# Kernel optimization log

Measured on AMD Instinct MI355X. Metric: run time of the kernel, lower is better.

The kernel has to match this reference:

```python
import jax, jax.numpy as jnp
import numpy as np

HIDDEN = 2048
N_HEADS = 16
N_KV = 4
HEAD_DIM = 128
THETA = 500000.0
FREQ_ALLOC = 20  # t section; h = w = (HEAD_DIM//2 - 20)//2 = 22
T = 2048


def setup_inputs() -> dict:
    key = jax.random.key(0)
    k1, k2, k3, k4 = jax.random.split(key, 4)
    positions = jax.random.randint(k1, (3, T), 0, 1024, dtype=jnp.int32)
    hidden_states = jax.random.normal(k2, (T, HIDDEN), dtype=jnp.float32)
    w_qkv = jax.random.normal(k3, (HIDDEN, (N_HEADS + 2 * N_KV) * HEAD_DIM), dtype=jnp.float32) * 0.02
    w_o = jax.random.normal(k4, (N_HEADS * HEAD_DIM, HIDDEN), dtype=jnp.float32) * 0.02
    return {"positions": positions, "hidden_states": hidden_states, "w_qkv": w_qkv, "w_o": w_o}


def _mrope_cos_sin(positions):
    # standard rope table evaluated at positions: cos/sin each [3, T, HEAD_DIM//2]
    inv_freq = 1.0 / (THETA ** (jnp.arange(0, HEAD_DIM, 2, dtype=jnp.float32) / HEAD_DIM))
    freqs = positions.astype(jnp.float32)[..., None] * inv_freq
    cos, sin = jnp.cos(freqs), jnp.sin(freqs)
    sh = (HEAD_DIM // 2 - FREQ_ALLOC) // 2  # 22

    def section(c):
        c_t = c[0, :, -FREQ_ALLOC:]          # time dims from t-positions
        c_h = c[1, :, 0:2 * sh:2]            # even low-freq dims from h-positions
        c_w = c[2, :, 1:2 * sh:2]            # odd low-freq dims from w-positions
        c_hw = jnp.stack([c_h, c_w], axis=-1).reshape(c_h.shape[0], 2 * sh)
        return jnp.concatenate([c_hw, c_t], axis=-1)  # [T, HEAD_DIM//2]

    return section(cos), section(sin)


def _rotate_interleaved(x, cos, sin):
    # is_neox_style=False: even/odd interleaved rotation. x: [T, H, HEAD_DIM]
    x1, x2 = x[..., 0::2], x[..., 1::2]
    c, s = cos[:, None, :], sin[:, None, :]
    o1 = x1 * c - x2 * s
    o2 = x2 * c + x1 * s
    return jnp.stack([o1, o2], axis=-1).reshape(x.shape)


def reference(positions, hidden_states, w_qkv, w_o):
    q_size = N_HEADS * HEAD_DIM
    kv_size = N_KV * HEAD_DIM
    qkv = hidden_states @ w_qkv  # [T, 3072]
    q = qkv[:, :q_size].reshape(T, N_HEADS, HEAD_DIM)
    k = qkv[:, q_size:q_size + kv_size].reshape(T, N_KV, HEAD_DIM)
    v = qkv[:, q_size + kv_size:].reshape(T, N_KV, HEAD_DIM)

    cos, sin = _mrope_cos_sin(positions)
    q = _rotate_interleaved(q, cos, sin)
    k = _rotate_interleaved(k, cos, sin)

    # GQA causal attention
    rep = N_HEADS // N_KV
    kr = jnp.repeat(k, rep, axis=1)  # [T, N_HEADS, D]
    vr = jnp.repeat(v, rep, axis=1)
    scale = HEAD_DIM ** -0.5
    scores = jnp.einsum('qhd,khd->hqk', q, kr) * scale
    causal = jnp.tril(jnp.ones((T, T), dtype=bool))
    scores = jnp.where(causal[None], scores, jnp.finfo(scores.dtype).min)
    attn = jax.nn.softmax(scores, axis=-1)
    out = jnp.einsum('hqk,khd->qhd', attn, vr).reshape(T, N_HEADS * HEAD_DIM)
    return out @ w_o
```

## Files before the change

kernel.cpp:

```cpp
#include <hip/hip_runtime.h>
#include <math.h>

#define T 2048
#define HIDDEN 2048
#define NH 16
#define NKV 4
#define HD 128
#define QKV_N 3072
#define Q_SIZE 2048
#define KV_SIZE 512

typedef __attribute__((ext_vector_type(8))) short short8;
typedef __attribute__((ext_vector_type(4))) short short4v;
typedef __attribute__((ext_vector_type(4))) float floatx4;

__device__ __forceinline__ unsigned short f2bf(float f) {
    union { float f; unsigned int u; } v; v.f = f;
    unsigned int u = v.u;
    u += 0x7fffu + ((u >> 16) & 1u);
    return (unsigned short)(u >> 16);
}

__device__ __forceinline__ void gload_lds16(const unsigned short* g, unsigned short* l) {
    __builtin_amdgcn_global_load_lds((const __attribute__((address_space(1))) unsigned int*)g,
                                     (__attribute__((address_space(3))) unsigned int*)l, 16, 0, 0);
}

__global__ __launch_bounds__(256) void prep_misc(const float* __restrict__ hidden,
                                                 const float* __restrict__ w_qkv,
                                                 const float* __restrict__ w_o,
                                                 const int* __restrict__ positions,
                                                 unsigned short* __restrict__ hb,
                                                 unsigned short* __restrict__ wqt,
                                                 unsigned short* __restrict__ wot,
                                                 float* __restrict__ cosT,
                                                 float* __restrict__ sinT) {
    __shared__ float tile[32][33];
    const int b = blockIdx.x;
    const int tid = threadIdx.x;
    const int tx = tid & 31, ty = tid >> 5;

    if (b < 4096) {
        int i = (b * 256 + tid) * 4;
        float4 v = *(const float4*)(hidden + i);
        hb[i]     = f2bf(v.x);
        hb[i + 1] = f2bf(v.y);
        hb[i + 2] = f2bf(v.z);
        hb[i + 3] = f2bf(v.w);
    } else if (b < 10240) {
        int idx = b - 4096;
        int c0 = (idx % 96) * 32, r0 = (idx / 96) * 32;
#pragma unroll
        for (int i = 0; i < 4; ++i)
            tile[ty + i * 8][tx] = w_qkv[(long)(r0 + ty + i * 8) * QKV_N + c0 + tx];
        __syncthreads();
#pragma unroll
        for (int i = 0; i < 4; ++i)
            wqt[(long)(c0 + ty + i * 8) * HIDDEN + r0 + tx] = f2bf(tile[tx][ty + i * 8]);
    } else if (b < 14336) {
        int idx = b - 10240;
        int c0 = (idx % 64) * 32, r0 = (idx / 64) * 32;
#pragma unroll
        for (int i = 0; i < 4; ++i)
            tile[ty + i * 8][tx] = w_o[(long)(r0 + ty + i * 8) * HIDDEN + c0 + tx];
        __syncthreads();
#pragma unroll
        for (int i = 0; i < 4; ++i)
            wot[(long)(c0 + ty + i * 8) * HIDDEN + r0 + tx] = f2bf(tile[tx][ty + i * 8]);
    } else {
        int idx = b - 14336;
        int t = idx * 4 + (tid >> 6);
        int j = tid & 63;
        int row = (j >= 44) ? 0 : ((j & 1) ? 2 : 1);
        int pos = positions[row * T + t];
        float invf = exp2f((float)j * -0.29580571f);
        float ang = (float)pos * invf;
        cosT[t * 64 + j] = cosf(ang);
        sinT[t * 64 + j] = sinf(ang);
    }
}

__global__ __launch_bounds__(256) void gemm_qkv(const unsigned short* __restrict__ A,
                                                const unsigned short* __restrict__ B,
                                                const float* __restrict__ cosT,
                                                const float* __restrict__ sinT,
                                                unsigned short* __restrict__ qb,
                                                unsigned short* __restrict__ kb,
                                                unsigned short* __restrict__ vt) {
    __shared__ __align__(16) unsigned short As[2][64 * 64];
    __shared__ __align__(16) unsigned short Bs[2][128 * 64];
    const int K = HIDDEN;
    const int tid = threadIdx.x;
    const int wv = tid >> 6;
    const int lane = tid & 63;
    const int m = lane & 15, qd = lane >> 4;
    const unsigned short* Ab = A + (long)(blockIdx.x * 64) * K;
    const unsigned short* Bb = B + (long)(blockIdx.y * 128) * K;

    floatx4 acc[4][2];
#pragma unroll
    for (int i = 0; i < 4; ++i)
#pragma unroll
        for (int j = 0; j < 2; ++j) acc[i][j] = (floatx4){0.f, 0.f, 0.f, 0.f};

#define QKV_STAGE(buf, k0)                                                                   \
    do {                                                                                     \
        _Pragma("unroll") for (int i_ = 0; i_ < 2; ++i_) {                                   \
            int s_ = i_ * 256 + tid, r_ = s_ >> 3, c_ = (s_ & 7) ^ (r_ & 7);                 \
            gload_lds16(Ab + (long)r_ * K + (k0) + c_ * 8, &As[buf][i_ * 2048 + wv * 512]);  \
        }                                                                                    \
        _Pragma("unroll") for (int i_ = 0; i_ < 4; ++i_) {                                   \
            int s_ = i_ * 256 + tid, r_ = s_ >> 3, c_ = (s_ & 7) ^ (r_ & 7);                 \
            gload_lds16(Bb + (long)r_ * K + (k0) + c_ * 8, &Bs[buf][i_ * 2048 + wv * 512]);  \
        }                                                                                    \
    } while (0)

    QKV_STAGE(0, 0);
    int cur = 0;
    for (int k0 = 0; k0 < K; k0 += 64) {
        __syncthreads();
        if (k0 + 64 < K) QKV_STAGE(cur ^ 1, k0 + 64);
#pragma unroll
        for (int kk = 0; kk < 2; ++kk) {
            const int rch = ((kk * 4 + qd) ^ (m & 7)) * 8;
            short8 a[4], b[2];
#pragma unroll
            for (int i = 0; i < 4; ++i) a[i] = *(const short8*)&As[cur][(i * 16 + m) * 64 + rch];
#pragma unroll
            for (int j = 0; j < 2; ++j) b[j] = *(const short8*)&Bs[cur][(wv * 32 + j * 16 + m) * 64 + rch];
#pragma unroll
            for (int i = 0; i < 4; ++i)
#pragma unroll
                for (int j = 0; j < 2; ++j)
                    acc[i][j] = __builtin_amdgcn_mfma_f32_16x16x32_bf16(a[i], b[j], acc[i][j], 0, 0, 0);
        }
        cur ^= 1;
    }
#undef QKV_STAGE

    const int by = blockIdx.y;
    if (by < 20) {
        const float sgn = (m & 1) ? 1.f : -1.f;
        const float qscale = 0.08838834764831845f;
#pragma unroll
        for (int i = 0; i < 4; ++i) {
#pragma unroll
            for (int r = 0; r < 4; ++r) {
                const int t = blockIdx.x * 64 + i * 16 + qd * 4 + r;
                const float* ct = cosT + t * 64;
                const float* st = sinT + t * 64;
#pragma unroll
                for (int j = 0; j < 2; ++j) {
                    const int cq = wv * 32 + j * 16 + m;
                    const int j2 = cq >> 1;
                    float val = acc[i][j][r];
                    float prt = __shfl_xor(val, 1);
                    float o = val * ct[j2] + sgn * prt * st[j2];
                    const int col = by * 128 + cq;
                    if (by < 16) qb[(long)t * Q_SIZE + col] = f2bf(o * qscale);
                    else         kb[(long)t * KV_SIZE + (col - 2048)] = f2bf(o);
                }
            }
        }
    } else {
        const int g = by - 20;
#pragma unroll
        for (int i = 0; i < 4; ++i)
#pragma unroll
            for (int j = 0; j < 2; ++j) {
                const int d = wv * 32 + j * 16 + m;
                const int t0 = blockIdx.x * 64 + i * 16 + qd * 4;
                unsigned short o4[4];
#pragma unroll
                for (int r = 0; r < 4; ++r) o4[r] = f2bf(acc[i][j][r]);
                *(short4v*)&vt[((long)g * HD + d) * T + t0] = *(short4v*)o4;
            }
    }
}

__global__ __launch_bounds__(256) void gemm_out(const unsigned short* __restrict__ A,
                                                const unsigned short* __restrict__ B,
                                                float* __restrict__ C,
                                                int K, int ldc) {
    __shared__ __align__(16) unsigned short As[2][64 * 64];
    __shared__ __align__(16) unsigned short Bs[2][128 * 64];
    const int tid = threadIdx.x;
    const int wv = tid >> 6;
    const int lane = tid & 63;
    const int m = lane & 15, qd = lane >> 4;
    const unsigned short* Ab = A + (long)(blockIdx.x * 64) * K;
    const unsigned short* Bb = B + (long)(blockIdx.y * 128) * K;

    floatx4 acc[4][2];
#pragma unroll
    for (int i = 0; i < 4; ++i)
#pragma unroll
        for (int j = 0; j < 2; ++j) acc[i][j] = (floatx4){0.f, 0.f, 0.f, 0.f};

#define OUT_STAGE(buf, k0)                                                                   \
    do {                                                                                     \
        _Pragma("unroll") for (int i_ = 0; i_ < 2; ++i_) {                                   \
            int s_ = i_ * 256 + tid, r_ = s_ >> 3, c_ = (s_ & 7) ^ (r_ & 7);                 \
            gload_lds16(Ab + (long)r_ * K + (k0) + c_ * 8, &As[buf][i_ * 2048 + wv * 512]);  \
        }                                                                                    \
        _Pragma("unroll") for (int i_ = 0; i_ < 4; ++i_) {                                   \
            int s_ = i_ * 256 + tid, r_ = s_ >> 3, c_ = (s_ & 7) ^ (r_ & 7);                 \
            gload_lds16(Bb + (long)r_ * K + (k0) + c_ * 8, &Bs[buf][i_ * 2048 + wv * 512]);  \
        }                                                                                    \
    } while (0)

    OUT_STAGE(0, 0);
    int cur = 0;
    for (int k0 = 0; k0 < K; k0 += 64) {
        __syncthreads();
        if (k0 + 64 < K) OUT_STAGE(cur ^ 1, k0 + 64);
#pragma unroll
        for (int kk = 0; kk < 2; ++kk) {
            const int rch = ((kk * 4 + qd) ^ (m & 7)) * 8;
            short8 a[4], b[2];
#pragma unroll
            for (int i = 0; i < 4; ++i) a[i] = *(const short8*)&As[cur][(i * 16 + m) * 64 + rch];
#pragma unroll
            for (int j = 0; j < 2; ++j) b[j] = *(const short8*)&Bs[cur][(wv * 32 + j * 16 + m) * 64 + rch];
#pragma unroll
            for (int i = 0; i < 4; ++i)
#pragma unroll
                for (int j = 0; j < 2; ++j)
                    acc[i][j] = __builtin_amdgcn_mfma_f32_16x16x32_bf16(a[i], b[j], acc[i][j], 0, 0, 0);
        }
        cur ^= 1;
    }
#undef OUT_STAGE

#pragma unroll
    for (int i = 0; i < 4; ++i)
#pragma unroll
        for (int j = 0; j < 2; ++j)
#pragma unroll
            for (int r = 0; r < 4; ++r)
                C[(long)(blockIdx.x * 64 + i * 16 + qd * 4 + r) * ldc +
                  blockIdx.y * 128 + wv * 32 + j * 16 + m] = acc[i][j][r];
}

__global__ __launch_bounds__(256, 2) void flash_attn(const unsigned short* __restrict__ qb,
                                                     const unsigned short* __restrict__ kb,
                                                     const unsigned short* __restrict__ vt,
                                                     float* __restrict__ Opart,
                                                     float* __restrict__ MLpart) {
    __shared__ __align__(16) unsigned short Kbuf[2][64 * 128];
    __shared__ __align__(16) unsigned short Vbuf[128 * 64];
    __shared__ __align__(16) unsigned short Pls[4][32 * 72];

    const int tid = threadIdx.x;
    const int wv = tid >> 6;
    const int lane = tid & 63;
    const int m = lane & 15;
    const int qd = lane >> 4;

    const int bx = blockIdx.x;
    const int c_ = bx & 255;
    const int hi = bx >> 8;
    const int h = c_ >> 4;
    const int j_ = c_ & 15;
    const int qt = hi ? (j_ >> 1) : (15 - (j_ >> 1));
    const int half = j_ & 1;
    const int g = h >> 2;
    unsigned short* myP = Pls[wv];

    const int n0 = qt + 1;
    const int jt0 = half ? n0 : 0;
    const int jt1 = half ? 2 * qt + 2 : n0;
    const int q0 = qt * 128;

    short8 aq[2][4];
#pragma unroll
    for (int s = 0; s < 2; ++s)
#pragma unroll
        for (int kk = 0; kk < 4; ++kk)
            aq[s][kk] = *(const short8*)(qb + (long)(q0 + s * 64 + wv * 16 + m) * Q_SIZE +
                                         h * HD + kk * 32 + qd * 8);

    floatx4 acc_o[2][8];
#pragma unroll
    for (int s = 0; s < 2; ++s)
#pragma unroll
        for (int nb = 0; nb < 8; ++nb) acc_o[s][nb] = (floatx4){0.f, 0.f, 0.f, 0.f};
    float mrow[2] = {-1e30f, -1e30f};
    float lrow[2] = {0.f, 0.f};

#pragma unroll
    for (int i = 0; i < 4; ++i) {
        int s_ = i * 256 + tid;
        int r = s_ >> 4, c = (s_ & 15) ^ (r & 15);
        gload_lds16(kb + (long)(jt0 * 64 + r) * KV_SIZE + g * HD + c * 8,
                    &Kbuf[0][i * 2048 + wv * 512]);
    }
    int cur = 0;
    for (int jt = jt0; jt < jt1; ++jt) {
        __syncthreads();

        if (jt + 1 < jt1) {
#pragma unroll
            for (int i = 0; i < 4; ++i) {
                int s_ = i * 256 + tid;
                int r = s_ >> 4, c = (s_ & 15) ^ (r & 15);
                gload_lds16(kb + (long)((jt + 1) * 64 + r) * KV_SIZE + g * HD + c * 8,
                            &Kbuf[cur ^ 1][i * 2048 + wv * 512]);
            }
        }
#pragma unroll
        for (int i = 0; i < 4; ++i) {
            int s_ = i * 256 + tid;
            int r = s_ >> 3, c = (s_ & 7) ^ (r & 7);
            gload_lds16(vt + ((long)g * HD + r) * T + jt * 64 + c * 8,
                        &Vbuf[i * 2048 + wv * 512]);
        }

        floatx4 acc_s[2][4];
#pragma unroll
        for (int s = 0; s < 2; ++s)
#pragma unroll
            for (int c = 0; c < 4; ++c) acc_s[s][c] = (floatx4){0.f, 0.f, 0.f, 0.f};
#pragma unroll
        for (int kk = 0; kk < 4; ++kk) {
#pragma unroll
            for (int c = 0; c < 4; ++c) {
                short8 ak = *(const short8*)&Kbuf[cur][(c * 16 + m) * 128 +
                                                       (((4 * kk + qd) ^ m) * 8)];
                acc_s[0][c] = __builtin_amdgcn_mfma_f32_16x16x32_bf16(ak, aq[0][kk], acc_s[0][c], 0, 0, 0);
                acc_s[1][c] = __builtin_amdgcn_mfma_f32_16x16x32_bf16(ak, aq[1][kk], acc_s[1][c], 0, 0, 0);
            }
        }

#pragma unroll
        for (int s = 0; s < 2; ++s) {
            const int dg = 2 * qt + s;
            if (jt >= dg) {
                const bool full = (jt > dg);
#pragma unroll
                for (int c = 0; c < 4; ++c)
#pragma unroll
                    for (int r = 0; r < 4; ++r)
                        if (full || (c * 16 + qd * 4 + r > wv * 16 + m)) acc_s[s][c][r] = -1e30f;
            }
            float mx = acc_s[s][0][0];
#pragma unroll
            for (int c = 0; c < 4; ++c)
#pragma unroll
                for (int r = 0; r < 4; ++r) mx = fmaxf(mx, acc_s[s][c][r]);
            mx = fmaxf(mx, __shfl_xor(mx, 16));
            mx = fmaxf(mx, __shfl_xor(mx, 32));
            float mnew = fmaxf(mrow[s], mx);
            float alpha = __expf(mrow[s] - mnew);
            mrow[s] = mnew;

            float pv[4][4];
            float lsum = 0.f;
#pragma unroll
            for (int c = 0; c < 4; ++c)
#pragma unroll
                for (int r = 0; r < 4; ++r) {
                    pv[c][r] = __expf(acc_s[s][c][r] - mnew);
                    lsum += pv[c][r];
                }
            lsum += __shfl_xor(lsum, 16);
            lsum += __shfl_xor(lsum, 32);
            lrow[s] = lrow[s] * alpha + lsum;
#pragma unroll
            for (int nb = 0; nb < 8; ++nb)
#pragma unroll
                for (int r = 0; r < 4; ++r) acc_o[s][nb][r] *= alpha;
#pragma unroll
            for (int c = 0; c < 4; ++c) {
                short4v pk = {(short)f2bf(pv[c][0]), (short)f2bf(pv[c][1]),
                              (short)f2bf(pv[c][2]), (short)f2bf(pv[c][3])};
                *(short4v*)&myP[(s * 16 + m) * 72 + c * 16 + qd * 4] = pk;
            }
        }

        __syncthreads();

#pragma unroll
        for (int kk = 0; kk < 2; ++kk) {
            short8 pa0 = *(const short8*)&myP[m * 72 + kk * 32 + qd * 8];
            short8 pa1 = *(const short8*)&myP[(16 + m) * 72 + kk * 32 + qd * 8];
#pragma unroll
            for (int nb = 0; nb < 8; ++nb) {
                short8 av = *(const short8*)&Vbuf[(nb * 16 + m) * 64 +
                                                  (((4 * kk + qd) ^ (m & 7)) * 8)];
                acc_o[0][nb] = __builtin_amdgcn_mfma_f32_16x16x32_bf16(av, pa0, acc_o[0][nb], 0, 0, 0);
                acc_o[1][nb] = __builtin_amdgcn_mfma_f32_16x16x32_bf16(av, pa1, acc_o[1][nb], 0, 0, 0);
            }
        }
        cur ^= 1;
    }

    const int unit = (h * 16 + qt) * 2 + half;
#pragma unroll
    for (int s = 0; s < 2; ++s) {
        const long rb = (long)unit * 128 + s * 64 + wv * 16 + m;
#pragma unroll
        for (int nb = 0; nb < 8; ++nb)
            *(floatx4*)&Opart[rb * 128 + nb * 16 + qd * 4] = acc_o[s][nb];
        if (qd == 0) {
            MLpart[rb * 2]     = mrow[s];
            MLpart[rb * 2 + 1] = lrow[s];
        }
    }
}

__global__ __launch_bounds__(256) void attn_combine(const float* __restrict__ Opart,
                                                    const float* __restrict__ MLpart,
                                                    unsigned short* __restrict__ ab) {
    const int tid = threadIdx.x;
    const int q = blockIdx.x * 16 + (tid >> 4);
    const int h = blockIdx.y;
    const int d0 = (tid & 15) * 8;
    const int qt = q >> 7, lr = q & 127;
    const long r0 = ((long)(h * 16 + qt) * 2) * 128 + lr;
    const long r1 = r0 + 128;
    float m0 = MLpart[r0 * 2], l0 = MLpart[r0 * 2 + 1];
    float m1 = MLpart[r1 * 2], l1 = MLpart[r1 * 2 + 1];
    float M = fmaxf(m0, m1);
    float a0 = __expf(m0 - M), a1 = __expf(m1 - M);
    float inv = 1.f / (l0 * a0 + l1 * a1);
    const float* O0 = Opart + r0 * 128 + d0;
    const float* O1 = Opart + r1 * 128 + d0;
    unsigned short outv[8];
#pragma unroll
    for (int j = 0; j < 8; j += 4) {
        float4 x0 = *(const float4*)(O0 + j);
        float4 x1 = *(const float4*)(O1 + j);
        outv[j]     = f2bf((x0.x * a0 + x1.x * a1) * inv);
        outv[j + 1] = f2bf((x0.y * a0 + x1.y * a1) * inv);
        outv[j + 2] = f2bf((x0.z * a0 + x1.z * a1) * inv);
        outv[j + 3] = f2bf((x0.w * a0 + x1.w * a1) * inv);
    }
    *(short8*)&ab[(long)q * Q_SIZE + h * HD + d0] = *(short8*)outv;
}

extern "C" void kernel_launch(void* const* d_in, const int* in_sizes, int n_in,
                              void* d_out, int out_size, void* d_ws, size_t ws_size,
                              hipStream_t stream) {
    const int* positions = (const int*)d_in[0];
    const float* hidden  = (const float*)d_in[1];
    const float* w_qkv   = (const float*)d_in[2];
    const float* w_o     = (const float*)d_in[3];
    float* out = (float*)d_out;

    char* p = (char*)d_ws;
    auto alloc = [&](size_t bytes) { char* r = p; p += (bytes + 255) & ~(size_t)255; return r; };
    float* cosT = (float*)alloc((size_t)T * 64 * 4);
    float* sinT = (float*)alloc((size_t)T * 64 * 4);
    unsigned short* hb  = (unsigned short*)alloc((size_t)T * HIDDEN * 2);
    unsigned short* wqt = (unsigned short*)alloc((size_t)QKV_N * HIDDEN * 2);
    unsigned short* wot = (unsigned short*)alloc((size_t)HIDDEN * HIDDEN * 2);
    unsigned short* qb  = (unsigned short*)alloc((size_t)T * Q_SIZE * 2);
    unsigned short* kb  = (unsigned short*)alloc((size_t)T * KV_SIZE * 2);
    unsigned short* vt  = (unsigned short*)alloc((size_t)T * KV_SIZE * 2);
    unsigned short* ab  = (unsigned short*)alloc((size_t)T * Q_SIZE * 2);
    float* Opart  = (float*)alloc((size_t)512 * 128 * 128 * 4);
    float* MLpart = (float*)alloc((size_t)512 * 128 * 2 * 4);

    prep_misc<<<dim3(14848), 256, 0, stream>>>(hidden, w_qkv, w_o, positions,
                                               hb, wqt, wot, cosT, sinT);
    gemm_qkv<<<dim3(T / 64, QKV_N / 128), 256, 0, stream>>>(hb, wqt, cosT, sinT, qb, kb, vt);
    flash_attn<<<dim3(512), 256, 0, stream>>>(qb, kb, vt, Opart, MLpart);
    attn_combine<<<dim3(T / 16, NH), 256, 0, stream>>>(Opart, MLpart, ab);
    gemm_out<<<dim3(T / 64, HIDDEN / 128), 256, 0, stream>>>(ab, wot, out, Q_SIZE, HIDDEN);
}
```

Before: 220.4 us.

## Triple-buffer GEMMs with 32x32 MFMA tiles and raw vmcnt barriers

```diff
diff --git a/kernel.cpp b/kernel.cpp
--- a/kernel.cpp
+++ b/kernel.cpp
@@ -13,6 +13,15 @@
 typedef __attribute__((ext_vector_type(8))) short short8;
 typedef __attribute__((ext_vector_type(4))) short short4v;
 typedef __attribute__((ext_vector_type(4))) float floatx4;
+typedef __attribute__((ext_vector_type(16))) float floatx16;
+
+#define VMCNT(N) asm volatile("s_waitcnt vmcnt(" #N ")" ::: "memory")
+#define LGKMCNT0 asm volatile("s_waitcnt lgkmcnt(0)" ::: "memory")
+#define BARRIER_RAW()                          \
+    do {                                       \
+        __builtin_amdgcn_s_barrier();          \
+        asm volatile("" ::: "memory");         \
+    } while (0)
 
 __device__ __forceinline__ unsigned short f2bf(float f) {
     union { float f; unsigned int u; } v; v.f = f;
@@ -80,101 +89,127 @@
     }
 }
 
-__global__ __launch_bounds__(256) void gemm_qkv(const unsigned short* __restrict__ A,
+__global__ __launch_bounds__(384) void gemm_qkv(const unsigned short* __restrict__ A,
                                                 const unsigned short* __restrict__ B,
                                                 const float* __restrict__ cosT,
                                                 const float* __restrict__ sinT,
                                                 unsigned short* __restrict__ qb,
                                                 unsigned short* __restrict__ kb,
                                                 unsigned short* __restrict__ vt) {
-    __shared__ __align__(16) unsigned short As[2][64 * 64];
-    __shared__ __align__(16) unsigned short Bs[2][128 * 64];
-    const int K = HIDDEN;
+    __shared__ __align__(16) unsigned short Ls[3][320 * 64];
     const int tid = threadIdx.x;
     const int wv = tid >> 6;
     const int lane = tid & 63;
-    const int m = lane & 15, qd = lane >> 4;
-    const unsigned short* Ab = A + (long)(blockIdx.x * 64) * K;
-    const unsigned short* Bb = B + (long)(blockIdx.y * 128) * K;
-
-    floatx4 acc[4][2];
-#pragma unroll
-    for (int i = 0; i < 4; ++i)
-#pragma unroll
-        for (int j = 0; j < 2; ++j) acc[i][j] = (floatx4){0.f, 0.f, 0.f, 0.f};
-
-#define QKV_STAGE(buf, k0)                                                                   \
-    do {                                                                                     \
-        _Pragma("unroll") for (int i_ = 0; i_ < 2; ++i_) {                                   \
-            int s_ = i_ * 256 + tid, r_ = s_ >> 3, c_ = (s_ & 7) ^ (r_ & 7);                 \
-            gload_lds16(Ab + (long)r_ * K + (k0) + c_ * 8, &As[buf][i_ * 2048 + wv * 512]);  \
-        }                                                                                    \
-        _Pragma("unroll") for (int i_ = 0; i_ < 4; ++i_) {                                   \
-            int s_ = i_ * 256 + tid, r_ = s_ >> 3, c_ = (s_ & 7) ^ (r_ & 7);                 \
-            gload_lds16(Bb + (long)r_ * K + (k0) + c_ * 8, &Bs[buf][i_ * 2048 + wv * 512]);  \
-        }                                                                                    \
+    const int l31 = lane & 31;
+    const int hi = lane >> 5;
+    const int wr = wv / 3;
+    const int wc = wv - wr * 3;
+    const int by = blockIdx.x;
+    const int bx = blockIdx.y;
+    const unsigned short* Ab = A + (long)(bx * 128) * HIDDEN;
+    const unsigned short* Bb = B + (long)(by * 192) * HIDDEN;
+
+    floatx16 acc[2][2];
+#pragma unroll
+    for (int i = 0; i < 2; ++i)
+#pragma unroll
+        for (int j = 0; j < 2; ++j) acc[i][j] = (floatx16)0.0f;
+
+#define QKV_STAGE(bufidx, k0)                                                          \
+    do {                                                                               \
+        unsigned short* lb_ = &Ls[bufidx][0];                                          \
+        for (int q_ = wv; q_ < 40; q_ += 6) {                                          \
+            int s_ = q_ * 64 + lane;                                                   \
+            int r_ = s_ >> 3;                                                          \
+            int c_ = (s_ & 7) ^ (r_ & 7);                                              \
+            const unsigned short* src_ = (q_ < 16)                                     \
+                ? (Ab + (long)r_ * HIDDEN + (k0) + c_ * 8)                             \
+                : (Bb + (long)(r_ - 128) * HIDDEN + (k0) + c_ * 8);                    \
+            gload_lds16(src_, lb_ + q_ * 512);                                         \
+        }                                                                              \
     } while (0)
 
     QKV_STAGE(0, 0);
+    QKV_STAGE(1, 64);
     int cur = 0;
-    for (int k0 = 0; k0 < K; k0 += 64) {
-        __syncthreads();
-        if (k0 + 64 < K) QKV_STAGE(cur ^ 1, k0 + 64);
-#pragma unroll
-        for (int kk = 0; kk < 2; ++kk) {
-            const int rch = ((kk * 4 + qd) ^ (m & 7)) * 8;
-            short8 a[4], b[2];
-#pragma unroll
-            for (int i = 0; i < 4; ++i) a[i] = *(const short8*)&As[cur][(i * 16 + m) * 64 + rch];
-#pragma unroll
-            for (int j = 0; j < 2; ++j) b[j] = *(const short8*)&Bs[cur][(wv * 32 + j * 16 + m) * 64 + rch];
-#pragma unroll
-            for (int i = 0; i < 4; ++i)
+    const int arow0 = wr * 64 + l31;
+    const int brow0 = 128 + wc * 64 + l31;
+#pragma unroll 1
+    for (int t = 0; t < 32; ++t) {
+        if (t < 31) {
+            if (wv < 4) VMCNT(7); else VMCNT(6);
+        } else {
+            VMCNT(0);
+        }
+        BARRIER_RAW();
+        if (t + 2 < 32) {
+            int nb = cur + 2; if (nb >= 3) nb -= 3;
+            QKV_STAGE(nb, (t + 2) * 64);
+        }
+        const unsigned short* lb = &Ls[cur][0];
+#pragma unroll
+        for (int kk = 0; kk < 4; ++kk) {
+            const int ck = kk * 2 + hi;
+            short8 a[2], b[2];
+#pragma unroll
+            for (int i = 0; i < 2; ++i) {
+                const int row = arow0 + i * 32;
+                a[i] = *(const short8*)&lb[row * 64 + ((ck ^ (row & 7)) << 3)];
+            }
+#pragma unroll
+            for (int j = 0; j < 2; ++j) {
+                const int row = brow0 + j * 32;
+                b[j] = *(const short8*)&lb[row * 64 + ((ck ^ (row & 7)) << 3)];
+            }
+#pragma unroll
+            for (int i = 0; i < 2; ++i)
 #pragma unroll
                 for (int j = 0; j < 2; ++j)
-                    acc[i][j] = __builtin_amdgcn_mfma_f32_16x16x32_bf16(a[i], b[j], acc[i][j], 0, 0, 0);
-        }
-        cur ^= 1;
+                    acc[i][j] = __builtin_amdgcn_mfma_f32_32x32x16_bf16(a[i], b[j], acc[i][j], 0, 0, 0);
+        }
+        LGKMCNT0;
+        cur = (cur == 2) ? 0 : cur + 1;
     }
 #undef QKV_STAGE
 
-    const int by = blockIdx.y;
-    if (by < 20) {
-        const float sgn = (m & 1) ? 1.f : -1.f;
-        const float qscale = 0.08838834764831845f;
-#pragma unroll
-        for (int i = 0; i < 4; ++i) {
-#pragma unroll
-            for (int r = 0; r < 4; ++r) {
-                const int t = blockIdx.x * 64 + i * 16 + qd * 4 + r;
-                const float* ct = cosT + t * 64;
-                const float* st = sinT + t * 64;
-#pragma unroll
-                for (int j = 0; j < 2; ++j) {
-                    const int cq = wv * 32 + j * 16 + m;
-                    const int j2 = cq >> 1;
-                    float val = acc[i][j][r];
-                    float prt = __shfl_xor(val, 1);
-                    float o = val * ct[j2] + sgn * prt * st[j2];
-                    const int col = by * 128 + cq;
-                    if (by < 16) qb[(long)t * Q_SIZE + col] = f2bf(o * qscale);
-                    else         kb[(long)t * KV_SIZE + (col - 2048)] = f2bf(o);
+    const float qscale = 0.08838834764831845f;
+#pragma unroll
+    for (int i = 0; i < 2; ++i) {
+#pragma unroll
+        for (int j = 0; j < 2; ++j) {
+            const int colbase = by * 192 + wc * 64 + j * 32;
+            const int col = colbase + l31;
+            const int trow0 = bx * 128 + wr * 64 + i * 32 + 4 * hi;
+            if (colbase < Q_SIZE + KV_SIZE) {
+                const float sgn = (col & 1) ? 1.f : -1.f;
+                const int j2 = (col & 127) >> 1;
+#pragma unroll
+                for (int h = 0; h < 4; ++h) {
+#pragma unroll
+                    for (int r = 0; r < 4; ++r) {
+                        const int tt = trow0 + 8 * h + r;
+                        float val = acc[i][j][h * 4 + r];
+                        float prt = __shfl_xor(val, 1);
+                        float o = val * cosT[tt * 64 + j2] + sgn * prt * sinT[tt * 64 + j2];
+                        if (colbase < Q_SIZE)
+                            qb[(long)tt * Q_SIZE + col] = f2bf(o * qscale);
+                        else
+                            kb[(long)tt * KV_SIZE + (col - Q_SIZE)] = f2bf(o);
+                    }
                 }
-            }
-        }
-    } else {
-        const int g = by - 20;
-#pragma unroll
-        for (int i = 0; i < 4; ++i)
-#pragma unroll
-            for (int j = 0; j < 2; ++j) {
-                const int d = wv * 32 + j * 16 + m;
-                const int t0 = blockIdx.x * 64 + i * 16 + qd * 4;
-                unsigned short o4[4];
-#pragma unroll
-                for (int r = 0; r < 4; ++r) o4[r] = f2bf(acc[i][j][r]);
-                *(short4v*)&vt[((long)g * HD + d) * T + t0] = *(short4v*)o4;
-            }
+            } else {
+                const int vcol = col - (Q_SIZE + KV_SIZE);
+                const int g = vcol >> 7, d = vcol & 127;
+#pragma unroll
+                for (int h = 0; h < 4; ++h) {
+                    const int t0 = trow0 + 8 * h;
+                    unsigned short o4[4];
+#pragma unroll
+                    for (int r = 0; r < 4; ++r) o4[r] = f2bf(acc[i][j][h * 4 + r]);
+                    *(short4v*)&vt[((long)g * HD + d) * T + t0] = *(short4v*)o4;
+                }
+            }
+        }
     }
 }
 
@@ -182,64 +217,91 @@
                                                 const unsigned short* __restrict__ B,
                                                 float* __restrict__ C,
                                                 int K, int ldc) {
-    __shared__ __align__(16) unsigned short As[2][64 * 64];
-    __shared__ __align__(16) unsigned short Bs[2][128 * 64];
+    __shared__ __align__(16) unsigned short Ls[3][256 * 64];
     const int tid = threadIdx.x;
     const int wv = tid >> 6;
     const int lane = tid & 63;
-    const int m = lane & 15, qd = lane >> 4;
-    const unsigned short* Ab = A + (long)(blockIdx.x * 64) * K;
-    const unsigned short* Bb = B + (long)(blockIdx.y * 128) * K;
-
-    floatx4 acc[4][2];
-#pragma unroll
-    for (int i = 0; i < 4; ++i)
-#pragma unroll
-        for (int j = 0; j < 2; ++j) acc[i][j] = (floatx4){0.f, 0.f, 0.f, 0.f};
-
-#define OUT_STAGE(buf, k0)                                                                   \
-    do {                                                                                     \
-        _Pragma("unroll") for (int i_ = 0; i_ < 2; ++i_) {                                   \
-            int s_ = i_ * 256 + tid, r_ = s_ >> 3, c_ = (s_ & 7) ^ (r_ & 7);                 \
-            gload_lds16(Ab + (long)r_ * K + (k0) + c_ * 8, &As[buf][i_ * 2048 + wv * 512]);  \
-        }                                                                                    \
-        _Pragma("unroll") for (int i_ = 0; i_ < 4; ++i_) {                                   \
-            int s_ = i_ * 256 + tid, r_ = s_ >> 3, c_ = (s_ & 7) ^ (r_ & 7);                 \
-            gload_lds16(Bb + (long)r_ * K + (k0) + c_ * 8, &Bs[buf][i_ * 2048 + wv * 512]);  \
-        }                                                                                    \
+    const int l31 = lane & 31;
+    const int hi = lane >> 5;
+    const int wr = wv >> 1, wc = wv & 1;
+    const int by = blockIdx.x;
+    const int bx = blockIdx.y;
+    const unsigned short* Ab = A + (long)(bx * 128) * K;
+    const unsigned short* Bb = B + (long)(by * 128) * K;
+
+    floatx16 acc[2][2];
+#pragma unroll
+    for (int i = 0; i < 2; ++i)
+#pragma unroll
+        for (int j = 0; j < 2; ++j) acc[i][j] = (floatx16)0.0f;
+
+#define OUT_STAGE(bufidx, k0)                                                          \
+    do {                                                                               \
+        unsigned short* lb_ = &Ls[bufidx][0];                                          \
+        _Pragma("unroll") for (int qq_ = 0; qq_ < 8; ++qq_) {                          \
+            int q_ = qq_ * 4 + wv;                                                     \
+            int s_ = q_ * 64 + lane;                                                   \
+            int r_ = s_ >> 3;                                                          \
+            int c_ = (s_ & 7) ^ (r_ & 7);                                              \
+            const unsigned short* src_ = (q_ < 16)                                     \
+                ? (Ab + (long)r_ * K + (k0) + c_ * 8)                                  \
+                : (Bb + (long)(r_ - 128) * K + (k0) + c_ * 8);                         \
+            gload_lds16(src_, lb_ + q_ * 512);                                         \
+        }                                                                              \
     } while (0)
 
+    const int NT = K >> 6;
     OUT_STAGE(0, 0);
+    OUT_STAGE(1, 64);
     int cur = 0;
-    for (int k0 = 0; k0 < K; k0 += 64) {
-        __syncthreads();
-        if (k0 + 64 < K) OUT_STAGE(cur ^ 1, k0 + 64);
-#pragma unroll
-        for (int kk = 0; kk < 2; ++kk) {
-            const int rch = ((kk * 4 + qd) ^ (m & 7)) * 8;
-            short8 a[4], b[2];
-#pragma unroll
-            for (int i = 0; i < 4; ++i) a[i] = *(const short8*)&As[cur][(i * 16 + m) * 64 + rch];
-#pragma unroll
-            for (int j = 0; j < 2; ++j) b[j] = *(const short8*)&Bs[cur][(wv * 32 + j * 16 + m) * 64 + rch];
-#pragma unroll
-            for (int i = 0; i < 4; ++i)
+    const int arow0 = wr * 64 + l31;
+    const int brow0 = 128 + wc * 64 + l31;
+#pragma unroll 1
+    for (int t = 0; t < NT; ++t) {
+        if (t < NT - 1) VMCNT(8); else VMCNT(0);
+        BARRIER_RAW();
+        if (t + 2 < NT) {
+            int nb = cur + 2; if (nb >= 3) nb -= 3;
+            OUT_STAGE(nb, (t + 2) * 64);
+        }
+        const unsigned short* lb = &Ls[cur][0];
+#pragma unroll
+        for (int kk = 0; kk < 4; ++kk) {
+            const int ck = kk * 2 + hi;
+            short8 a[2], b[2];
+#pragma unroll
+            for (int i = 0; i < 2; ++i) {
+                const int row = arow0 + i * 32;
+                a[i] = *(const short8*)&lb[row * 64 + ((ck ^ (row & 7)) << 3)];
+            }
+#pragma unroll
+            for (int j = 0; j < 2; ++j) {
+                const int row = brow0 + j * 32;
+                b[j] = *(const short8*)&lb[row * 64 + ((ck ^ (row & 7)) << 3)];
+            }
+#pragma unroll
+            for (int i = 0; i < 2; ++i)
 #pragma unroll
                 for (int j = 0; j < 2; ++j)
-                    acc[i][j] = __builtin_amdgcn_mfma_f32_16x16x32_bf16(a[i], b[j], acc[i][j], 0, 0, 0);
-        }
-        cur ^= 1;
+                    acc[i][j] = __builtin_amdgcn_mfma_f32_32x32x16_bf16(a[i], b[j], acc[i][j], 0, 0, 0);
+        }
+        LGKMCNT0;
+        cur = (cur == 2) ? 0 : cur + 1;
     }
 #undef OUT_STAGE
 
 #pragma unroll
-    for (int i = 0; i < 4; ++i)
-#pragma unroll
-        for (int j = 0; j < 2; ++j)
-#pragma unroll
-            for (int r = 0; r < 4; ++r)
-                C[(long)(blockIdx.x * 64 + i * 16 + qd * 4 + r) * ldc +
-                  blockIdx.y * 128 + wv * 32 + j * 16 + m] = acc[i][j][r];
+    for (int i = 0; i < 2; ++i)
+#pragma unroll
+        for (int j = 0; j < 2; ++j) {
+            const long rbase = (long)(bx * 128 + wr * 64 + i * 32 + 4 * hi);
+            const int cbase = by * 128 + wc * 64 + j * 32 + l31;
+#pragma unroll
+            for (int h = 0; h < 4; ++h)
+#pragma unroll
+                for (int r = 0; r < 4; ++r)
+                    C[(rbase + 8 * h + r) * ldc + cbase] = acc[i][j][h * 4 + r];
+        }
 }
 
 __global__ __launch_bounds__(256, 2) void flash_attn(const unsigned short* __restrict__ qb,
@@ -297,9 +359,18 @@
     }
     int cur = 0;
     for (int jt = jt0; jt < jt1; ++jt) {
-        __syncthreads();
-
-        if (jt + 1 < jt1) {
+        VMCNT(0);
+        BARRIER_RAW();
+
+#pragma unroll
+        for (int i = 0; i < 4; ++i) {
+            int s_ = i * 256 + tid;
+            int r = s_ >> 3, c = (s_ & 7) ^ (r & 7);
+            gload_lds16(vt + ((long)g * HD + r) * T + jt * 64 + c * 8,
+                        &Vbuf[i * 2048 + wv * 512]);
+        }
+        const bool pk = (jt + 1 < jt1);
+        if (pk) {
 #pragma unroll
             for (int i = 0; i < 4; ++i) {
                 int s_ = i * 256 + tid;
@@ -307,13 +378,6 @@
                 gload_lds16(kb + (long)((jt + 1) * 64 + r) * KV_SIZE + g * HD + c * 8,
                             &Kbuf[cur ^ 1][i * 2048 + wv * 512]);
             }
-        }
-#pragma unroll
-        for (int i = 0; i < 4; ++i) {
-            int s_ = i * 256 + tid;
-            int r = s_ >> 3, c = (s_ & 7) ^ (r & 7);
-            gload_lds16(vt + ((long)g * HD + r) * T + jt * 64 + c * 8,
-                        &Vbuf[i * 2048 + wv * 512]);
         }
 
         floatx4 acc_s[2][4];
@@ -372,13 +436,14 @@
                 for (int r = 0; r < 4; ++r) acc_o[s][nb][r] *= alpha;
 #pragma unroll
             for (int c = 0; c < 4; ++c) {
-                short4v pk = {(short)f2bf(pv[c][0]), (short)f2bf(pv[c][1]),
-                              (short)f2bf(pv[c][2]), (short)f2bf(pv[c][3])};
-                *(short4v*)&myP[(s * 16 + m) * 72 + c * 16 + qd * 4] = pk;
-            }
-        }
-
-        __syncthreads();
+                short4v pk2 = {(short)f2bf(pv[c][0]), (short)f2bf(pv[c][1]),
+                               (short)f2bf(pv[c][2]), (short)f2bf(pv[c][3])};
+                *(short4v*)&myP[(s * 16 + m) * 72 + c * 16 + qd * 4] = pk2;
+            }
+        }
+
+        if (pk) VMCNT(4); else VMCNT(0);
+        BARRIER_RAW();
 
 #pragma unroll
         for (int kk = 0; kk < 2; ++kk) {
@@ -392,6 +457,7 @@
                 acc_o[1][nb] = __builtin_amdgcn_mfma_f32_16x16x32_bf16(av, pa1, acc_o[1][nb], 0, 0, 0);
             }
         }
+        LGKMCNT0;
         cur ^= 1;
     }
 
@@ -464,8 +530,8 @@
 
     prep_misc<<<dim3(14848), 256, 0, stream>>>(hidden, w_qkv, w_o, positions,
                                                hb, wqt, wot, cosT, sinT);
-    gemm_qkv<<<dim3(T / 64, QKV_N / 128), 256, 0, stream>>>(hb, wqt, cosT, sinT, qb, kb, vt);
+    gemm_qkv<<<dim3(QKV_N / 192, T / 128), 384, 0, stream>>>(hb, wqt, cosT, sinT, qb, kb, vt);
     flash_attn<<<dim3(512), 256, 0, stream>>>(qb, kb, vt, Opart, MLpart);
     attn_combine<<<dim3(T / 16, NH), 256, 0, stream>>>(Opart, MLpart, ab);
-    gemm_out<<<dim3(T / 64, HIDDEN / 128), 256, 0, stream>>>(ab, wot, out, Q_SIZE, HIDDEN);
-}
+    gemm_out<<<dim3(HIDDEN / 128, T / 128), 256, 0, stream>>>(ab, wot, out, Q_SIZE, HIDDEN);
+}
```

Result: slower. 228.9 us (+3.9%).
